# Performance work log

Measured on AMD Instinct MI355X. Metric: run time of the kernel, lower is better.

## Reference

```python
import jax, jax.numpy as jnp
import numpy as np

N = 2
GRIDS = [(512, 512), (256, 256), (128, 128), (64, 64), (32, 32)]
STRIDES = [4, 8, 16, 32, 64]
SIZES = [32, 64, 128, 256, 512]
ASPECTS = (0.5, 1.0, 2.0)
A = len(ASPECTS)
IMG_H = IMG_W = 2048
PRE_NMS = 1000      # pre_nms_top_n['testing']
POST_NMS = 1000     # post_nms_top_n['testing']
NMS_THRESH = 0.7
SCORE_THRESH = 0.0
MIN_SIZE = 1e-3
BBOX_XFORM_CLIP = float(np.log(1000.0 / 16.0))  # torchvision BoxCoder clamp


def _make_anchors():
    """AnchorGenerator.grid_anchors for each level; returns list of [H*W*A, 4]."""
    ar = jnp.asarray(ASPECTS, jnp.float32)
    hr = jnp.sqrt(ar)
    wr = 1.0 / hr
    levels = []
    for (gh, gw), s, size in zip(GRIDS, STRIDES, SIZES):
        ws = wr * size
        hs = hr * size
        base = jnp.round(jnp.stack([-ws, -hs, ws, hs], 1) / 2.0)  # [A,4]
        sx = (jnp.arange(gw) * s).astype(jnp.float32)
        sy = (jnp.arange(gh) * s).astype(jnp.float32)
        yy, xx = jnp.meshgrid(sy, sx, indexing='ij')
        shifts = jnp.stack([xx.ravel(), yy.ravel(), xx.ravel(), yy.ravel()], 1)
        levels.append((shifts[:, None, :] + base[None, :, :]).reshape(-1, 4))
    return levels


def _flatten_obj(o):
    # permute_and_flatten with C=1: [N,A,H,W] -> [N, H*W*A]
    n, ac, h, w = o.shape
    return o.reshape(n, ac, 1, h, w).transpose(0, 3, 4, 1, 2).reshape(n, -1)


def _flatten_box(b):
    # permute_and_flatten with C=4: [N,A*4,H,W] -> [N, H*W*A, 4]
    n, a4, h, w = b.shape
    return b.reshape(n, a4 // 4, 4, h, w).transpose(0, 3, 4, 1, 2).reshape(n, -1, 4)


def _decode(deltas, anchors):
    # BoxCoder.decode with weights (1,1,1,1); deltas [N,M,4], anchors [M,4]
    wa = anchors[:, 2] - anchors[:, 0]
    ha = anchors[:, 3] - anchors[:, 1]
    cxa = anchors[:, 0] + 0.5 * wa
    cya = anchors[:, 1] + 0.5 * ha
    dx, dy = deltas[..., 0], deltas[..., 1]
    dw = jnp.minimum(deltas[..., 2], BBOX_XFORM_CLIP)
    dh = jnp.minimum(deltas[..., 3], BBOX_XFORM_CLIP)
    cx = dx * wa + cxa
    cy = dy * ha + cya
    w = jnp.exp(dw) * wa
    h = jnp.exp(dh) * ha
    return jnp.stack([cx - 0.5 * w, cy - 0.5 * h, cx + 0.5 * w, cy + 0.5 * h], -1)


def _nms_select(boxes, scores, n_out, thresh):
    """Greedy NMS returning fixed n_out (index, valid) pairs. boxes [K,4]."""
    area = jnp.maximum(boxes[:, 2] - boxes[:, 0], 0.0) * jnp.maximum(boxes[:, 3] - boxes[:, 1], 0.0)

    def step(s, _):
        i = jnp.argmax(s)
        valid = s[i] > -jnp.inf
        b = boxes[i]
        lt = jnp.maximum(boxes[:, :2], b[:2])
        rb = jnp.minimum(boxes[:, 2:], b[2:])
        wh = jnp.maximum(rb - lt, 0.0)
        inter = wh[:, 0] * wh[:, 1]
        iou = inter / (area + area[i] - inter + 1e-9)
        s = jnp.where(iou > thresh, -jnp.inf, s).at[i].set(-jnp.inf)
        return s, (i, valid)

    _, (idx, valid) = jax.lax.scan(step, scores, None, length=n_out)
    return idx, valid


def _rpn_forward(objs, dts):
    anchors = _make_anchors()
    b_all, s_all, l_all = [], [], []
    for li, (o, d, a) in enumerate(zip(objs, dts, anchors)):
        of = _flatten_obj(o)            # [N, HWA]
        df = _flatten_box(d)            # [N, HWA, 4]
        props = _decode(df, a)          # [N, HWA, 4]
        k = min(PRE_NMS, of.shape[1])
        ts, ti = jax.lax.top_k(of, k)   # top-k on raw objectness (per level)
        b_all.append(jnp.take_along_axis(props, ti[..., None], 1))
        s_all.append(ts)
        l_all.append(jnp.full((of.shape[0], k), float(li), jnp.float32))
    boxes = jnp.concatenate(b_all, 1)   # [N, K, 4]
    raw = jnp.concatenate(s_all, 1)     # [N, K]
    lvl = jnp.concatenate(l_all, 1)     # [N, K]

    def per_image(bx, rs, lv):
        sc = jax.nn.sigmoid(rs)
        x1 = jnp.clip(bx[:, 0], 0.0, IMG_W)
        y1 = jnp.clip(bx[:, 1], 0.0, IMG_H)
        x2 = jnp.clip(bx[:, 2], 0.0, IMG_W)
        y2 = jnp.clip(bx[:, 3], 0.0, IMG_H)
        bx = jnp.stack([x1, y1, x2, y2], 1)
        keep = ((x2 - x1) >= MIN_SIZE) & ((y2 - y1) >= MIN_SIZE) & (sc > SCORE_THRESH)
        ms = jnp.where(keep, sc, -jnp.inf)
        off = lv * (IMG_W + IMG_H + 1.0)  # batched_nms level offset
        idx, valid = _nms_select(jax.lax.stop_gradient(bx + off[:, None]),
                                 jax.lax.stop_gradient(ms), POST_NMS, NMS_THRESH)
        v = valid.astype(bx.dtype)
        ob = bx[idx] * v[:, None]
        os = sc[idx] * v
        return jnp.concatenate([ob, os[:, None]], 1)  # [POST_NMS, 5]

    return jax.vmap(per_image)(boxes, raw, lvl)       # [N, POST_NMS, 5]


def setup_inputs() -> dict:
    key = jax.random.key(0)
    ks = jax.random.split(key, 10)
    inp = {}
    for i, (gh, gw) in enumerate(GRIDS):
        inp[f"obj{i}"] = jax.random.normal(ks[i], (N, A, gh, gw), jnp.float32)
        inp[f"box{i}"] = jax.random.normal(ks[5 + i], (N, A * 4, gh, gw), jnp.float32) * 0.5
    return inp


def reference(obj0, obj1, obj2, obj3, obj4, box0, box1, box2, box3, box4):
    return _rpn_forward([obj0, obj1, obj2, obj3, obj4],
                        [box0, box1, box2, box3, box4])
```

## Files before the change

kernel.cpp:

```cpp
#include <hip/hip_runtime.h>
#include <cmath>

#pragma clang fp contract(off)

typedef unsigned int u32;
typedef unsigned short u16;
typedef unsigned long long u64;

#define K_PER_LVL 1000
#define KTOT 5000
#define NIMG 2
#define BINS 16384
#define BIN_SHIFT 18
#define SEGW (BINS / 256)
#define EQ_CAP 2048
#define ECAP 32768
#define LECAP 24576
#define CBUF 1024
#define RNK_IB 512
#define RNK_JB 250
#define RNK_NJ (KTOT / RNK_JB)
#define RNK_TILES 200
#define EDGE_TILES 820

__constant__ int c_LG[5] = {512, 256, 128, 64, 32};
__constant__ int c_LS[5] = {4, 8, 16, 32, 64};
__constant__ int c_LZ[5] = {32, 64, 128, 256, 512};
__constant__ int c_LM[5] = {786432, 196608, 49152, 12288, 3072};

struct Ptrs { const float* o[5]; const float* b[5]; };

__device__ inline u32 fkey(float f) {
    u32 u = __float_as_uint(f);
    return (u & 0x80000000u) ? ~u : (u | 0x80000000u);
}

__global__ __launch_bounds__(256) void k_zero(u32* __restrict__ z, int nwords) {
    int i = blockIdx.x * 256 + threadIdx.x;
    int stride = gridDim.x * 256;
    for (; i < nwords; i += stride) z[i] = 0;
}

__global__ __launch_bounds__(256) void k_hist(Ptrs P, u32* __restrict__ hist) {
    int p = blockIdx.y; int l = p % 5; int n = p / 5;
    int M4 = c_LM[l] >> 2;
    const float4* base = (const float4*)(P.o[l] + (size_t)n * c_LM[l]);
    __shared__ u32 lh[BINS];
    for (int i = threadIdx.x; i < BINS; i += 256) lh[i] = 0;
    __syncthreads();
    int stride = gridDim.x * 256;
    for (int i = blockIdx.x * 256 + threadIdx.x; i < M4; i += stride) {
        float4 v = base[i];
        atomicAdd(&lh[fkey(v.x) >> BIN_SHIFT], 1u);
        atomicAdd(&lh[fkey(v.y) >> BIN_SHIFT], 1u);
        atomicAdd(&lh[fkey(v.z) >> BIN_SHIFT], 1u);
        atomicAdd(&lh[fkey(v.w) >> BIN_SHIFT], 1u);
    }
    __syncthreads();
    for (int i = threadIdx.x; i < BINS; i += 256) {
        u32 c = lh[i];
        if (c) atomicAdd(&hist[p * BINS + i], c);
    }
}

__global__ __launch_bounds__(256) void k_resolve(const u32* __restrict__ hist,
                                                 int* __restrict__ binB, int* __restrict__ kneed,
                                                 int* __restrict__ g0) {
    int p = blockIdx.x, t = threadIdx.x;
    __shared__ u32 seg[256];
    __shared__ u32 tail[SEGW];
    __shared__ int sgS; __shared__ u32 GS;
    u32 s = 0;
    const u32* hb = hist + p * BINS;
    int base = t * SEGW;
    for (int q = 0; q < SEGW; ++q) s += hb[base + q];
    seg[t] = s;
    __syncthreads();
    if (t == 0) {
        u32 G = 0; int sg = 255;
        for (; sg > 0; --sg) {
            if (G + seg[sg] >= (u32)K_PER_LVL) break;
            G += seg[sg];
        }
        sgS = sg; GS = G;
    }
    __syncthreads();
    int sg = sgS;
    if (t < SEGW) tail[t] = hb[sg * SEGW + t];
    __syncthreads();
    if (t == 0) {
        u32 G = GS; int B = sg * SEGW;
        for (int b = SEGW - 1; b >= 0; --b) {
            u32 c = tail[b];
            if (G + c >= (u32)K_PER_LVL) { B = sg * SEGW + b; break; }
            G += c;
        }
        binB[p] = B;
        kneed[p] = K_PER_LVL - (int)G;
        g0[p] = (int)G;
    }
}

__global__ __launch_bounds__(256) void k_compact(Ptrs P, const int* __restrict__ binB,
                                                 u32* gcnt, u32* ecnt,
                                                 int* __restrict__ sel, u64* __restrict__ eq) {
    int p = blockIdx.y; int l = p % 5; int n = p / 5;
    int M4 = c_LM[l] >> 2; int gg = c_LM[l] / 3;
    const float4* base = (const float4*)(P.o[l] + (size_t)n * c_LM[l]);
    int B = binB[p];
    __shared__ u32 lsel[CBUF];
    __shared__ u64 leq[CBUF];
    __shared__ u32 cSel, cEq, baseSel, baseEq;
    if (threadIdx.x == 0) { cSel = 0; cEq = 0; }
    __syncthreads();
    int stride = gridDim.x * 256;
    for (int i4 = blockIdx.x * 256 + threadIdx.x; i4 < M4; i4 += stride) {
        float4 v = base[i4];
        float vv[4] = {v.x, v.y, v.z, v.w};
        #pragma unroll
        for (int q = 0; q < 4; ++q) {
            u32 k = fkey(vv[q]);
            int bin = (int)(k >> BIN_SHIFT);
            if (bin < B) continue;
            int i = i4 * 4 + q;
            int a = i / gg; int pix = i - a * gg; int m = pix * 3 + a;
            if (bin > B) {
                u32 t = atomicAdd(&cSel, 1u);
                if (t < CBUF) lsel[t] = (u32)m;
                else { u32 pos = atomicAdd(&gcnt[p], 1u); sel[p * K_PER_LVL + pos] = m; }
            } else {
                u64 pk = ((u64)k << 20) | (u64)(0xFFFFFu ^ (u32)m);
                u32 t = atomicAdd(&cEq, 1u);
                if (t < CBUF) leq[t] = pk;
                else { u32 e = atomicAdd(&ecnt[p], 1u); if (e < EQ_CAP) eq[(size_t)p * EQ_CAP + e] = pk; }
            }
        }
    }
    __syncthreads();
    if (threadIdx.x == 0) {
        u32 ns = cSel < CBUF ? cSel : CBUF;
        u32 ne = cEq < CBUF ? cEq : CBUF;
        baseSel = ns ? atomicAdd(&gcnt[p], ns) : 0u;
        baseEq  = ne ? atomicAdd(&ecnt[p], ne) : 0u;
    }
    __syncthreads();
    u32 ns = cSel < CBUF ? cSel : CBUF;
    u32 ne = cEq < CBUF ? cEq : CBUF;
    for (u32 i = threadIdx.x; i < ns; i += 256) sel[p * K_PER_LVL + baseSel + i] = (int)lsel[i];
    for (u32 i = threadIdx.x; i < ne; i += 256) {
        u32 slot = baseEq + i;
        if (slot < EQ_CAP) eq[(size_t)p * EQ_CAP + slot] = leq[i];
    }
}

__global__ __launch_bounds__(256) void k_eqsel(const u32* __restrict__ ecnt, const int* __restrict__ kneed,
                                               const int* __restrict__ g0,
                                               const u64* __restrict__ eq, int* __restrict__ sel) {
    int p = blockIdx.x, t = threadIdx.x;
    int E = (int)ecnt[p]; if (E > EQ_CAP) E = EQ_CAP;
    int KF = kneed[p]; int G0 = g0[p];
    __shared__ u64 a[EQ_CAP];
    for (int i = t; i < E; i += 256) a[i] = eq[(size_t)p * EQ_CAP + i];
    __syncthreads();
    u64 mine[8]; int rk[8];
    #pragma unroll
    for (int q = 0; q < 8; ++q) {
        int i = t + q * 256;
        mine[q] = (i < E) ? a[i] : 0ULL;
        rk[q] = 0;
    }
    for (int j = 0; j < E; ++j) {
        u64 v = a[j];
        #pragma unroll
        for (int q = 0; q < 8; ++q) rk[q] += (v > mine[q]) ? 1 : 0;
    }
    #pragma unroll
    for (int q = 0; q < 8; ++q) {
        int i = t + q * 256;
        if (i < E && rk[q] < KF) {
            int m = (int)(0xFFFFFu ^ (u32)(mine[q] & 0xFFFFFu));
            sel[p * K_PER_LVL + G0 + rk[q]] = m;
        }
    }
}

__global__ void k_feat(Ptrs P, const int* __restrict__ sel, u64* __restrict__ key64,
                       float* __restrict__ csc, float* __restrict__ cbox, float* __restrict__ cobox) {
    int tid = blockIdx.x * 256 + threadIdx.x;
    if (tid >= NIMG * KTOT) return;
    int p = tid / K_PER_LVL, s = tid - p * K_PER_LVL;
    int n = p / 5, l = p % 5;
    int G = c_LG[l], S = c_LS[l], Z = c_LZ[l];
    int gg = G * G;
    int m = sel[p * K_PER_LVL + s];
    int a = m % 3; int pix = m / 3; int h = pix / G; int w = pix - h * G;

    const float ars[3] = {0.5f, 1.0f, 2.0f};
    float ar = ars[a];
    float hr = sqrtf(ar), wr = 1.0f / hr;
    float wsz = wr * (float)Z, hsz = hr * (float)Z;
    float bx1 = rintf(-0.5f * wsz), by1 = rintf(-0.5f * hsz);
    float bx2 = rintf(0.5f * wsz),  by2 = rintf(0.5f * hsz);
    float sx = (float)(w * S), sy = (float)(h * S);
    float ax1 = sx + bx1, ay1 = sy + by1, ax2 = sx + bx2, ay2 = sy + by2;
    float wa = ax2 - ax1, ha = ay2 - ay1;
    float cxa = ax1 + 0.5f * wa, cya = ay1 + 0.5f * ha;

    const float* bb = P.b[l] + (size_t)n * 12 * gg;
    float dx = bb[(a * 4 + 0) * gg + pix];
    float dy = bb[(a * 4 + 1) * gg + pix];
    const float CLIPV = 4.135166556742356f;
    float dw = fminf(bb[(a * 4 + 2) * gg + pix], CLIPV);
    float dh = fminf(bb[(a * 4 + 3) * gg + pix], CLIPV);
    float cx = dx * wa + cxa, cy = dy * ha + cya;
    float ww = expf(dw) * wa, hh = expf(dh) * ha;
    float x1 = cx - 0.5f * ww, y1 = cy - 0.5f * hh;
    float x2 = cx + 0.5f * ww, y2 = cy + 0.5f * hh;
    x1 = fminf(fmaxf(x1, 0.f), 2048.f);
    y1 = fminf(fmaxf(y1, 0.f), 2048.f);
    x2 = fminf(fmaxf(x2, 0.f), 2048.f);
    y2 = fminf(fmaxf(y2, 0.f), 2048.f);

    float raw = P.o[l][(size_t)n * 3 * gg + a * gg + pix];
    float sc = 1.0f / (1.0f + expf(-raw));
    bool keep = (x2 - x1 >= 1e-3f) && (y2 - y1 >= 1e-3f) && (sc > 0.0f);

    int slot = n * KTOT + l * K_PER_LVL + s;
    u32 tb = ((u32)l << 20) | (u32)m;
    u32 kk = keep ? fkey(raw) : 0u;
    key64[slot] = ((u64)kk << 23) | (u64)(tb ^ 0x7FFFFFu);

    csc[slot] = keep ? sc : -INFINITY;
    cbox[slot * 4 + 0] = x1; cbox[slot * 4 + 1] = y1;
    cbox[slot * 4 + 2] = x2; cbox[slot * 4 + 3] = y2;
    float off = 4097.0f * (float)l;
    cobox[slot * 4 + 0] = x1 + off; cobox[slot * 4 + 1] = y1 + off;
    cobox[slot * 4 + 2] = x2 + off; cobox[slot * 4 + 3] = y2 + off;
}

__global__ __launch_bounds__(256) void k_redge(const u64* __restrict__ key64, u32* __restrict__ rpart,
                                               const float* __restrict__ cobox,
                                               u32* __restrict__ gE, u32* __restrict__ gPairs) {
    int n = blockIdx.y;
    int x = blockIdx.x;
    __shared__ u64 kj[RNK_JB];
    __shared__ float cb[64][4];
    if (x < RNK_TILES) {
        int i0 = (x / 20) * RNK_IB;
        int j0 = (x % 20) * RNK_JB;
        const u64* kb = key64 + (size_t)n * KTOT;
        for (int t = threadIdx.x; t < RNK_JB; t += 256) kj[t] = kb[j0 + t];
        __syncthreads();
        int i1 = i0 + threadIdx.x, i2 = i1 + 256;
        u64 k1 = (i1 < KTOT) ? kb[i1] : ~0ULL;
        u64 k2 = (i2 < KTOT) ? kb[i2] : ~0ULL;
        u32 r1 = 0, r2 = 0;
        #pragma unroll 10
        for (int j = 0; j < RNK_JB; ++j) {
            u64 v = kj[j];
            r1 += (v > k1) ? 1u : 0u;
            r2 += (v > k2) ? 1u : 0u;
        }
        u32* rp = rpart + (size_t)(x % 20) * (NIMG * KTOT) + n * KTOT;
        if (i1 < KTOT) rp[i1] = r1;
        if (i2 < KTOT) rp[i2] = r2;
        return;
    }
    int e = x - RNK_TILES, bi = 0;
    while (true) { int c = 79 - 4 * bi; if (e < c) break; e -= c; ++bi; }
    int bj = 4 * bi + e;
    int i = bi * 256 + threadIdx.x;
    int j0 = bj * 64;
    if (threadIdx.x < 64) {
        int jl = j0 + threadIdx.x;
        if (jl < KTOT) {
            cb[threadIdx.x][0] = cobox[(size_t)(n * KTOT + jl) * 4 + 0];
            cb[threadIdx.x][1] = cobox[(size_t)(n * KTOT + jl) * 4 + 1];
            cb[threadIdx.x][2] = cobox[(size_t)(n * KTOT + jl) * 4 + 2];
            cb[threadIdx.x][3] = cobox[(size_t)(n * KTOT + jl) * 4 + 3];
        } else {
            cb[threadIdx.x][0] = 0.f; cb[threadIdx.x][1] = 0.f;
            cb[threadIdx.x][2] = 0.f; cb[threadIdx.x][3] = 0.f;
        }
    }
    __syncthreads();
    if (i >= KTOT) return;
    float x1 = cobox[(size_t)(n * KTOT + i) * 4 + 0];
    float y1 = cobox[(size_t)(n * KTOT + i) * 4 + 1];
    float x2 = cobox[(size_t)(n * KTOT + i) * 4 + 2];
    float y2 = cobox[(size_t)(n * KTOT + i) * 4 + 3];
    float areai = fmaxf(x2 - x1, 0.f) * fmaxf(y2 - y1, 0.f);
    int lim = KTOT - j0; if (lim > 64) lim = 64;
    for (int jj = 0; jj < lim; ++jj) {
        int j = j0 + jj;
        if (j <= i) continue;
        float bx1 = cb[jj][0], by1 = cb[jj][1], bx2 = cb[jj][2], by2 = cb[jj][3];
        float areaj = fmaxf(bx2 - bx1, 0.f) * fmaxf(by2 - by1, 0.f);
        float ltx = fmaxf(x1, bx1), lty = fmaxf(y1, by1);
        float rbx = fminf(x2, bx2), rby = fminf(y2, by2);
        float iw = fmaxf(rbx - ltx, 0.f), ih = fmaxf(rby - lty, 0.f);
        float inter = iw * ih;
        float iou = inter / (areai + areaj - inter + 1e-9f);
        if (iou > 0.7f) {
            u32 pos = atomicAdd(&gE[n], 1u);
            if (pos < ECAP) gPairs[(size_t)n * ECAP + pos] = ((u32)i << 13) | (u32)j;
        }
    }
}

__global__ __launch_bounds__(256) void k_scat(const u32* __restrict__ rpart, const float* __restrict__ csc,
                       const float* __restrict__ cbox,
                       float* __restrict__ ssc, float* __restrict__ sbox, u32* __restrict__ rankArr) {
    int n = blockIdx.y;
    int i = blockIdx.x * 256 + threadIdx.x;
    if (i >= KTOT) return;
    int idx = n * KTOT + i;
    u32 rank = 0;
    #pragma unroll
    for (int jb = 0; jb < RNK_NJ; ++jb) rank += rpart[(size_t)jb * (NIMG * KTOT) + idx];
    rankArr[idx] = rank;
    int src = idx, dst = n * KTOT + (int)rank;
    ssc[dst] = csc[src];
    sbox[dst * 4 + 0] = cbox[src * 4 + 0]; sbox[dst * 4 + 1] = cbox[src * 4 + 1];
    sbox[dst * 4 + 2] = cbox[src * 4 + 2]; sbox[dst * 4 + 3] = cbox[src * 4 + 3];
}

__global__ __launch_bounds__(256, 1) void k_nms(const float* __restrict__ ssc,
                      const float* __restrict__ sbox, const u32* __restrict__ rankArr,
                      const u32* __restrict__ gE, const u32* __restrict__ gPairs,
                      u16* __restrict__ gEdges, float* __restrict__ out) {
    int n = blockIdx.x, tid = threadIdx.x;
    int lane = tid & 63, wv = tid >> 6;
    __shared__ u32 cnt[KTOT];
    __shared__ u32 offs[KTOT + 1];
    __shared__ u16 edges[LECAP];
    __shared__ u32 rem32[160];
    __shared__ u32 colLo[64], colHi[64];
    __shared__ u32 scanb[256];
    __shared__ int picksS;

    for (int i = tid; i < KTOT; i += 256) cnt[i] = 0;
    if (tid < 160) rem32[tid] = 0xFFFFFFFFu;
    __syncthreads();
    for (int w = wv; w < 79; w += 4) {
        int i = w * 64 + lane;
        bool dead = (i >= KTOT) || !(ssc[n * KTOT + i] > -INFINITY);
        u64 db = __ballot(dead);
        if (lane == 0) { rem32[2 * w] = (u32)db; rem32[2 * w + 1] = (u32)(db >> 32); }
    }
    __syncthreads();

    int E = (int)gE[n]; if (E > ECAP) E = ECAP;
    for (int k = tid; k < E; k += 256) {
        u32 p = gPairs[(size_t)n * ECAP + k];
        u32 ra = rankArr[n * KTOT + (p >> 13)], rb = rankArr[n * KTOT + (p & 0x1FFFu)];
        u32 src = ra < rb ? ra : rb;
        atomicAdd(&cnt[src], 1u);
    }
    __syncthreads();
    u32 s = 0; int base = tid * 20;
    if (tid < 250) for (int q = 0; q < 20; ++q) s += cnt[base + q];
    scanb[tid] = s;
    __syncthreads();
    for (int off = 1; off < 256; off <<= 1) {
        u32 v = (tid >= off) ? scanb[tid - off] : 0;
        __syncthreads();
        scanb[tid] += v;
        __syncthreads();
    }
    u32 tbase = (tid == 0) ? 0u : scanb[tid - 1];
    if (tid < 250) {
        u32 run = tbase;
        for (int q = 0; q < 20; ++q) { offs[base + q] = run; run += cnt[base + q]; }
    }
    if (tid == 0) offs[KTOT] = scanb[255];
    __syncthreads();
    for (int i = tid; i < KTOT; i += 256) cnt[i] = 0;
    __syncthreads();
    for (int k = tid; k < E; k += 256) {
        u32 p = gPairs[(size_t)n * ECAP + k];
        u32 ra = rankArr[n * KTOT + (p >> 13)], rb = rankArr[n * KTOT + (p & 0x1FFFu)];
        u32 src = ra < rb ? ra : rb, dst = ra < rb ? rb : ra;
        u32 slot = offs[src] + atomicAdd(&cnt[src], 1u);
        if (slot < LECAP) edges[slot] = (u16)dst;
        else gEdges[(size_t)n * ECAP + slot] = (u16)dst;
    }
    __syncthreads();

    if (wv == 0) {
        int picks = 0;
        for (int w = 0; w < 79 && picks < 1000; ++w) {
            u64 rw = ((u64)rem32[2 * w + 1] << 32) | rem32[2 * w];
            u64 alive = ~rw;
            if (alive == 0ULL) continue;
            int c = w * 64 + lane;
            bool amAlive = ((alive >> lane) & 1ULL) != 0ULL;
            int e0 = 0, e1 = 0;
            if (amAlive) { e0 = (int)offs[c]; e1 = (int)offs[c + 1]; }
            colLo[lane] = 0; colHi[lane] = 0;
            bool anyIntra = false;
            for (int k = e0; k < e1; ++k) {
                int dst = (k < LECAP) ? (int)edges[k] : (int)gEdges[(size_t)n * ECAP + k];
                if ((dst >> 6) == w) {
                    if (lane < 32) atomicOr(&colLo[dst & 63], 1u << lane);
                    else           atomicOr(&colHi[dst & 63], 1u << (lane - 32));
                    anyIntra = true;
                }
            }
            u64 cm;
            if (__ballot(anyIntra) == 0ULL) {
                cm = alive;
            } else {
                u64 col = ((u64)colHi[lane] << 32) | colLo[lane];
                cm = 0ULL;
                for (int e = 0; e < 64; ++e) {
                    if (!((alive >> e) & 1ULL)) continue;
                    u64 ce = __shfl(col, e);
                    if ((cm & ce) == 0ULL) cm |= (1ULL << e);
                }
            }
            int allowed = 1000 - picks;
            int ncom = __popcll(cm);
            while (ncom > allowed) { cm &= ~(1ULL << (63 - __clzll(cm))); --ncom; }
            if ((cm >> lane) & 1ULL) {
                int pos = picks + (int)__popcll(cm & ((1ULL << lane) - 1ULL));
                const float* bp = &sbox[(size_t)(n * KTOT + c) * 4];
                float* op = &out[(n * 1000 + pos) * 5];
                op[0] = bp[0]; op[1] = bp[1]; op[2] = bp[2]; op[3] = bp[3];
                op[4] = ssc[n * KTOT + c];
                for (int k = e0; k < e1; ++k) {
                    int dst = (k < LECAP) ? (int)edges[k] : (int)gEdges[(size_t)n * ECAP + k];
                    atomicOr(&rem32[dst >> 5], 1u << (dst & 31));
                }
            }
            picks += ncom;
        }
        if (lane == 0) picksS = picks;
    }
    __syncthreads();
    int picksF = picksS;
    int basec = (n * 1000 + picksF) * 5, cntz = (1000 - picksF) * 5;
    for (int t = tid; t < cntz; t += 256) out[basec + t] = 0.f;
}

constexpr size_t OFF_HIST   = 0;
constexpr size_t OFF_GCNT   = OFF_HIST + 10 * BINS * 4;
constexpr size_t OFF_ECNT   = OFF_GCNT + 64;
constexpr size_t OFF_GEC    = OFF_ECNT + 64;
constexpr size_t ZERO_WORDS = (10 * BINS * 4 + 192) / 4;
constexpr size_t OFF_BINB   = OFF_GEC + 64;
constexpr size_t OFF_KNEED  = OFF_BINB + 64;
constexpr size_t OFF_G0     = OFF_KNEED + 64;
constexpr size_t OFF_SEL    = OFF_G0 + 64;
constexpr size_t OFF_EQ     = OFF_SEL + 10 * K_PER_LVL * 4;
constexpr size_t OFF_KEY64  = OFF_EQ + (size_t)10 * EQ_CAP * 8;
constexpr size_t OFF_CSC    = OFF_KEY64 + (size_t)NIMG * KTOT * 8;
constexpr size_t OFF_CBOX   = OFF_CSC + (size_t)NIMG * KTOT * 4;
constexpr size_t OFF_COBOX  = OFF_CBOX + (size_t)NIMG * KTOT * 16;
constexpr size_t OFF_SSC    = OFF_COBOX + (size_t)NIMG * KTOT * 16;
constexpr size_t OFF_SBOX   = OFF_SSC + (size_t)NIMG * KTOT * 4;
constexpr size_t OFF_RANK   = OFF_SBOX + (size_t)NIMG * KTOT * 16;
constexpr size_t OFF_PAIRS  = OFF_RANK + (size_t)NIMG * KTOT * 4;
constexpr size_t OFF_ESPILL = OFF_PAIRS + (size_t)NIMG * ECAP * 4;
constexpr size_t OFF_RPART  = OFF_ESPILL + (size_t)NIMG * ECAP * 2;
constexpr size_t WS_NEEDED  = OFF_RPART + (size_t)RNK_NJ * NIMG * KTOT * 4;

extern "C" void kernel_launch(void* const* d_in, const int* in_sizes, int n_in,
                              void* d_out, int out_size, void* d_ws, size_t ws_size,
                              hipStream_t stream) {
    if (ws_size < WS_NEEDED) return;

    bool dictOrder = (in_sizes[1] > in_sizes[0]);
    Ptrs P;
    for (int l = 0; l < 5; ++l) {
        P.o[l] = (const float*)d_in[dictOrder ? (2 * l)     : l];
        P.b[l] = (const float*)d_in[dictOrder ? (2 * l + 1) : (5 + l)];
    }
    char* ws = (char*)d_ws;
    u32*   hist   = (u32*)(ws + OFF_HIST);
    u32*   gcnt   = (u32*)(ws + OFF_GCNT);
    u32*   ecnt   = (u32*)(ws + OFF_ECNT);
    u32*   gec    = (u32*)(ws + OFF_GEC);
    int*   binB   = (int*)(ws + OFF_BINB);
    int*   kneed  = (int*)(ws + OFF_KNEED);
    int*   g0     = (int*)(ws + OFF_G0);
    int*   sel    = (int*)(ws + OFF_SEL);
    u64*   eq     = (u64*)(ws + OFF_EQ);
    u64*   key64  = (u64*)(ws + OFF_KEY64);
    float* csc    = (float*)(ws + OFF_CSC);
    float* cbox   = (float*)(ws + OFF_CBOX);
    float* cobox  = (float*)(ws + OFF_COBOX);
    float* ssc    = (float*)(ws + OFF_SSC);
    float* sbox   = (float*)(ws + OFF_SBOX);
    u32*   rankA  = (u32*)(ws + OFF_RANK);
    u32*   pairs  = (u32*)(ws + OFF_PAIRS);
    u16*   espill = (u16*)(ws + OFF_ESPILL);
    u32*   rpart  = (u32*)(ws + OFF_RPART);
    float* out    = (float*)d_out;

    k_zero<<<dim3(64), 256, 0, stream>>>(hist, (int)ZERO_WORDS);
    k_hist<<<dim3(32, 10), 256, 0, stream>>>(P, hist);
    k_resolve<<<10, 256, 0, stream>>>(hist, binB, kneed, g0);
    k_compact<<<dim3(64, 10), 256, 0, stream>>>(P, binB, gcnt, ecnt, sel, eq);
    k_eqsel<<<10, 256, 0, stream>>>(ecnt, kneed, g0, eq, sel);
    k_feat<<<dim3((NIMG * KTOT + 255) / 256), 256, 0, stream>>>(P, sel, key64, csc, cbox, cobox);
    k_redge<<<dim3(RNK_TILES + EDGE_TILES, NIMG), 256, 0, stream>>>(key64, rpart, cobox, gec, pairs);
    k_scat<<<dim3((KTOT + 255) / 256, NIMG), 256, 0, stream>>>(rpart, csc, cbox, ssc, sbox, rankA);
    k_nms<<<NIMG, 256, 0, stream>>>(ssc, sbox, rankA, gec, pairs, espill, out);
}
```

Before: 199.3 us.

## Fuse RPN pipeline into one cooperative persistent kernel with grid syncs

Replaces the chain of nine kernel launches (zero, histogram, resolve, compact, equal-bin select, feature decode, rank/edge, scatter, NMS) with a single cooperative kernel of 256 blocks that steps through the stages separated by grid-wide barriers. Histogram work is remapped so slices are distributed per level in proportion to level size. The intent is to remove per-launch overhead and inter-kernel gaps on a pipeline made of many small stages. The cost is grid-sync latency, a fixed grid that may underuse the device in some stages, and shared-memory and occupancy limits from merging all stages into one kernel; the old multi-kernel path is kept as a fallback when cooperative launch is unavailable or fails.

```diff
diff --git a/kernel.cpp b/kernel.cpp
--- a/kernel.cpp
+++ b/kernel.cpp
@@ -1,7 +1,10 @@
 #include <hip/hip_runtime.h>
+#include <hip/hip_cooperative_groups.h>
 #include <cmath>
 
 #pragma clang fp contract(off)
+
+namespace cg = cooperative_groups;
 
 typedef unsigned int u32;
 typedef unsigned short u16;
@@ -22,6 +25,8 @@
 #define RNK_NJ (KTOT / RNK_JB)
 #define RNK_TILES 200
 #define EDGE_TILES 820
+#define NTILES (RNK_TILES + EDGE_TILES)
+#define GRID_ALL 256
 
 __constant__ int c_LG[5] = {512, 256, 128, 64, 32};
 __constant__ int c_LS[5] = {4, 8, 16, 32, 64};
@@ -30,169 +35,36 @@
 
 struct Ptrs { const float* o[5]; const float* b[5]; };
 
+struct Args {
+    Ptrs P;
+    u32* hist; u32* gcnt; u32* ecnt; u32* gec;
+    int* binB; int* kneed; int* g0; int* sel;
+    u64* eq; u64* key64;
+    float* csc; float* cbox; float* cobox;
+    u32* pairs; u16* espill; u32* rpart;
+    float* out;
+};
+
 __device__ inline u32 fkey(float f) {
     u32 u = __float_as_uint(f);
     return (u & 0x80000000u) ? ~u : (u | 0x80000000u);
 }
 
-__global__ __launch_bounds__(256) void k_zero(u32* __restrict__ z, int nwords) {
-    int i = blockIdx.x * 256 + threadIdx.x;
-    int stride = gridDim.x * 256;
-    for (; i < nwords; i += stride) z[i] = 0;
-}
-
-__global__ __launch_bounds__(256) void k_hist(Ptrs P, u32* __restrict__ hist) {
-    int p = blockIdx.y; int l = p % 5; int n = p / 5;
-    int M4 = c_LM[l] >> 2;
-    const float4* base = (const float4*)(P.o[l] + (size_t)n * c_LM[l]);
-    __shared__ u32 lh[BINS];
-    for (int i = threadIdx.x; i < BINS; i += 256) lh[i] = 0;
-    __syncthreads();
-    int stride = gridDim.x * 256;
-    for (int i = blockIdx.x * 256 + threadIdx.x; i < M4; i += stride) {
-        float4 v = base[i];
-        atomicAdd(&lh[fkey(v.x) >> BIN_SHIFT], 1u);
-        atomicAdd(&lh[fkey(v.y) >> BIN_SHIFT], 1u);
-        atomicAdd(&lh[fkey(v.z) >> BIN_SHIFT], 1u);
-        atomicAdd(&lh[fkey(v.w) >> BIN_SHIFT], 1u);
-    }
-    __syncthreads();
-    for (int i = threadIdx.x; i < BINS; i += 256) {
-        u32 c = lh[i];
-        if (c) atomicAdd(&hist[p * BINS + i], c);
-    }
-}
-
-__global__ __launch_bounds__(256) void k_resolve(const u32* __restrict__ hist,
-                                                 int* __restrict__ binB, int* __restrict__ kneed,
-                                                 int* __restrict__ g0) {
-    int p = blockIdx.x, t = threadIdx.x;
-    __shared__ u32 seg[256];
-    __shared__ u32 tail[SEGW];
-    __shared__ int sgS; __shared__ u32 GS;
-    u32 s = 0;
-    const u32* hb = hist + p * BINS;
-    int base = t * SEGW;
-    for (int q = 0; q < SEGW; ++q) s += hb[base + q];
-    seg[t] = s;
-    __syncthreads();
-    if (t == 0) {
-        u32 G = 0; int sg = 255;
-        for (; sg > 0; --sg) {
-            if (G + seg[sg] >= (u32)K_PER_LVL) break;
-            G += seg[sg];
-        }
-        sgS = sg; GS = G;
-    }
-    __syncthreads();
-    int sg = sgS;
-    if (t < SEGW) tail[t] = hb[sg * SEGW + t];
-    __syncthreads();
-    if (t == 0) {
-        u32 G = GS; int B = sg * SEGW;
-        for (int b = SEGW - 1; b >= 0; --b) {
-            u32 c = tail[b];
-            if (G + c >= (u32)K_PER_LVL) { B = sg * SEGW + b; break; }
-            G += c;
-        }
-        binB[p] = B;
-        kneed[p] = K_PER_LVL - (int)G;
-        g0[p] = (int)G;
-    }
-}
-
-__global__ __launch_bounds__(256) void k_compact(Ptrs P, const int* __restrict__ binB,
-                                                 u32* gcnt, u32* ecnt,
-                                                 int* __restrict__ sel, u64* __restrict__ eq) {
-    int p = blockIdx.y; int l = p % 5; int n = p / 5;
-    int M4 = c_LM[l] >> 2; int gg = c_LM[l] / 3;
-    const float4* base = (const float4*)(P.o[l] + (size_t)n * c_LM[l]);
-    int B = binB[p];
-    __shared__ u32 lsel[CBUF];
-    __shared__ u64 leq[CBUF];
-    __shared__ u32 cSel, cEq, baseSel, baseEq;
-    if (threadIdx.x == 0) { cSel = 0; cEq = 0; }
-    __syncthreads();
-    int stride = gridDim.x * 256;
-    for (int i4 = blockIdx.x * 256 + threadIdx.x; i4 < M4; i4 += stride) {
-        float4 v = base[i4];
-        float vv[4] = {v.x, v.y, v.z, v.w};
-        #pragma unroll
-        for (int q = 0; q < 4; ++q) {
-            u32 k = fkey(vv[q]);
-            int bin = (int)(k >> BIN_SHIFT);
-            if (bin < B) continue;
-            int i = i4 * 4 + q;
-            int a = i / gg; int pix = i - a * gg; int m = pix * 3 + a;
-            if (bin > B) {
-                u32 t = atomicAdd(&cSel, 1u);
-                if (t < CBUF) lsel[t] = (u32)m;
-                else { u32 pos = atomicAdd(&gcnt[p], 1u); sel[p * K_PER_LVL + pos] = m; }
-            } else {
-                u64 pk = ((u64)k << 20) | (u64)(0xFFFFFu ^ (u32)m);
-                u32 t = atomicAdd(&cEq, 1u);
-                if (t < CBUF) leq[t] = pk;
-                else { u32 e = atomicAdd(&ecnt[p], 1u); if (e < EQ_CAP) eq[(size_t)p * EQ_CAP + e] = pk; }
-            }
-        }
-    }
-    __syncthreads();
-    if (threadIdx.x == 0) {
-        u32 ns = cSel < CBUF ? cSel : CBUF;
-        u32 ne = cEq < CBUF ? cEq : CBUF;
-        baseSel = ns ? atomicAdd(&gcnt[p], ns) : 0u;
-        baseEq  = ne ? atomicAdd(&ecnt[p], ne) : 0u;
-    }
-    __syncthreads();
-    u32 ns = cSel < CBUF ? cSel : CBUF;
-    u32 ne = cEq < CBUF ? cEq : CBUF;
-    for (u32 i = threadIdx.x; i < ns; i += 256) sel[p * K_PER_LVL + baseSel + i] = (int)lsel[i];
-    for (u32 i = threadIdx.x; i < ne; i += 256) {
-        u32 slot = baseEq + i;
-        if (slot < EQ_CAP) eq[(size_t)p * EQ_CAP + slot] = leq[i];
-    }
-}
-
-__global__ __launch_bounds__(256) void k_eqsel(const u32* __restrict__ ecnt, const int* __restrict__ kneed,
-                                               const int* __restrict__ g0,
-                                               const u64* __restrict__ eq, int* __restrict__ sel) {
-    int p = blockIdx.x, t = threadIdx.x;
-    int E = (int)ecnt[p]; if (E > EQ_CAP) E = EQ_CAP;
-    int KF = kneed[p]; int G0 = g0[p];
-    __shared__ u64 a[EQ_CAP];
-    for (int i = t; i < E; i += 256) a[i] = eq[(size_t)p * EQ_CAP + i];
-    __syncthreads();
-    u64 mine[8]; int rk[8];
-    #pragma unroll
-    for (int q = 0; q < 8; ++q) {
-        int i = t + q * 256;
-        mine[q] = (i < E) ? a[i] : 0ULL;
-        rk[q] = 0;
-    }
-    for (int j = 0; j < E; ++j) {
-        u64 v = a[j];
-        #pragma unroll
-        for (int q = 0; q < 8; ++q) rk[q] += (v > mine[q]) ? 1 : 0;
-    }
-    #pragma unroll
-    for (int q = 0; q < 8; ++q) {
-        int i = t + q * 256;
-        if (i < E && rk[q] < KF) {
-            int m = (int)(0xFFFFFu ^ (u32)(mine[q] & 0xFFFFFu));
-            sel[p * K_PER_LVL + G0 + rk[q]] = m;
-        }
-    }
-}
-
-__global__ void k_feat(Ptrs P, const int* __restrict__ sel, u64* __restrict__ key64,
-                       float* __restrict__ csc, float* __restrict__ cbox, float* __restrict__ cobox) {
-    int tid = blockIdx.x * 256 + threadIdx.x;
-    if (tid >= NIMG * KTOT) return;
-    int p = tid / K_PER_LVL, s = tid - p * K_PER_LVL;
+__device__ inline void histMap(int b, int& p, int& sl, int& nsl) {
+    int n = b >> 7, r = b & 127;
+    int l, s0, c;
+    if (r < 94)       { l = 0; s0 = 0;   c = 94; }
+    else if (r < 118) { l = 1; s0 = 94;  c = 24; }
+    else if (r < 124) { l = 2; s0 = 118; c = 6;  }
+    else if (r < 126) { l = 3; s0 = 124; c = 2;  }
+    else              { l = 4; s0 = 126; c = 2;  }
+    p = n * 5 + l; sl = r - s0; nsl = c;
+}
+
+__device__ inline void featOneM(const Args& A, int p, int s, int m) {
     int n = p / 5, l = p % 5;
     int G = c_LG[l], S = c_LS[l], Z = c_LZ[l];
     int gg = G * G;
-    int m = sel[p * K_PER_LVL + s];
     int a = m % 3; int pix = m / 3; int h = pix / G; int w = pix - h * G;
 
     const float ars[3] = {0.5f, 1.0f, 2.0f};
@@ -206,7 +78,7 @@
     float wa = ax2 - ax1, ha = ay2 - ay1;
     float cxa = ax1 + 0.5f * wa, cya = ay1 + 0.5f * ha;
 
-    const float* bb = P.b[l] + (size_t)n * 12 * gg;
+    const float* bb = A.P.b[l] + (size_t)n * 12 * gg;
     float dx = bb[(a * 4 + 0) * gg + pix];
     float dy = bb[(a * 4 + 1) * gg + pix];
     const float CLIPV = 4.135166556742356f;
@@ -221,227 +93,41 @@
     x2 = fminf(fmaxf(x2, 0.f), 2048.f);
     y2 = fminf(fmaxf(y2, 0.f), 2048.f);
 
-    float raw = P.o[l][(size_t)n * 3 * gg + a * gg + pix];
+    float raw = A.P.o[l][(size_t)n * 3 * gg + a * gg + pix];
     float sc = 1.0f / (1.0f + expf(-raw));
     bool keep = (x2 - x1 >= 1e-3f) && (y2 - y1 >= 1e-3f) && (sc > 0.0f);
 
     int slot = n * KTOT + l * K_PER_LVL + s;
     u32 tb = ((u32)l << 20) | (u32)m;
     u32 kk = keep ? fkey(raw) : 0u;
-    key64[slot] = ((u64)kk << 23) | (u64)(tb ^ 0x7FFFFFu);
-
-    csc[slot] = keep ? sc : -INFINITY;
-    cbox[slot * 4 + 0] = x1; cbox[slot * 4 + 1] = y1;
-    cbox[slot * 4 + 2] = x2; cbox[slot * 4 + 3] = y2;
+    A.key64[slot] = ((u64)kk << 23) | (u64)(tb ^ 0x7FFFFFu);
+
+    A.csc[slot] = keep ? sc : -INFINITY;
+    A.cbox[slot * 4 + 0] = x1; A.cbox[slot * 4 + 1] = y1;
+    A.cbox[slot * 4 + 2] = x2; A.cbox[slot * 4 + 3] = y2;
     float off = 4097.0f * (float)l;
-    cobox[slot * 4 + 0] = x1 + off; cobox[slot * 4 + 1] = y1 + off;
-    cobox[slot * 4 + 2] = x2 + off; cobox[slot * 4 + 3] = y2 + off;
-}
-
-__global__ __launch_bounds__(256) void k_redge(const u64* __restrict__ key64, u32* __restrict__ rpart,
-                                               const float* __restrict__ cobox,
-                                               u32* __restrict__ gE, u32* __restrict__ gPairs) {
-    int n = blockIdx.y;
-    int x = blockIdx.x;
-    __shared__ u64 kj[RNK_JB];
-    __shared__ float cb[64][4];
-    if (x < RNK_TILES) {
-        int i0 = (x / 20) * RNK_IB;
-        int j0 = (x % 20) * RNK_JB;
-        const u64* kb = key64 + (size_t)n * KTOT;
-        for (int t = threadIdx.x; t < RNK_JB; t += 256) kj[t] = kb[j0 + t];
-        __syncthreads();
-        int i1 = i0 + threadIdx.x, i2 = i1 + 256;
-        u64 k1 = (i1 < KTOT) ? kb[i1] : ~0ULL;
-        u64 k2 = (i2 < KTOT) ? kb[i2] : ~0ULL;
-        u32 r1 = 0, r2 = 0;
-        #pragma unroll 10
-        for (int j = 0; j < RNK_JB; ++j) {
-            u64 v = kj[j];
-            r1 += (v > k1) ? 1u : 0u;
-            r2 += (v > k2) ? 1u : 0u;
-        }
-        u32* rp = rpart + (size_t)(x % 20) * (NIMG * KTOT) + n * KTOT;
-        if (i1 < KTOT) rp[i1] = r1;
-        if (i2 < KTOT) rp[i2] = r2;
-        return;
-    }
-    int e = x - RNK_TILES, bi = 0;
-    while (true) { int c = 79 - 4 * bi; if (e < c) break; e -= c; ++bi; }
-    int bj = 4 * bi + e;
-    int i = bi * 256 + threadIdx.x;
-    int j0 = bj * 64;
-    if (threadIdx.x < 64) {
-        int jl = j0 + threadIdx.x;
-        if (jl < KTOT) {
-            cb[threadIdx.x][0] = cobox[(size_t)(n * KTOT + jl) * 4 + 0];
-            cb[threadIdx.x][1] = cobox[(size_t)(n * KTOT + jl) * 4 + 1];
-            cb[threadIdx.x][2] = cobox[(size_t)(n * KTOT + jl) * 4 + 2];
-            cb[threadIdx.x][3] = cobox[(size_t)(n * KTOT + jl) * 4 + 3];
-        } else {
-            cb[threadIdx.x][0] = 0.f; cb[threadIdx.x][1] = 0.f;
-            cb[threadIdx.x][2] = 0.f; cb[threadIdx.x][3] = 0.f;
-        }
-    }
-    __syncthreads();
-    if (i >= KTOT) return;
-    float x1 = cobox[(size_t)(n * KTOT + i) * 4 + 0];
-    float y1 = cobox[(size_t)(n * KTOT + i) * 4 + 1];
-    float x2 = cobox[(size_t)(n * KTOT + i) * 4 + 2];
-    float y2 = cobox[(size_t)(n * KTOT + i) * 4 + 3];
-    float areai = fmaxf(x2 - x1, 0.f) * fmaxf(y2 - y1, 0.f);
-    int lim = KTOT - j0; if (lim > 64) lim = 64;
-    for (int jj = 0; jj < lim; ++jj) {
-        int j = j0 + jj;
-        if (j <= i) continue;
-        float bx1 = cb[jj][0], by1 = cb[jj][1], bx2 = cb[jj][2], by2 = cb[jj][3];
-        float areaj = fmaxf(bx2 - bx1, 0.f) * fmaxf(by2 - by1, 0.f);
-        float ltx = fmaxf(x1, bx1), lty = fmaxf(y1, by1);
-        float rbx = fminf(x2, bx2), rby = fminf(y2, by2);
-        float iw = fmaxf(rbx - ltx, 0.f), ih = fmaxf(rby - lty, 0.f);
-        float inter = iw * ih;
-        float iou = inter / (areai + areaj - inter + 1e-9f);
-        if (iou > 0.7f) {
-            u32 pos = atomicAdd(&gE[n], 1u);
-            if (pos < ECAP) gPairs[(size_t)n * ECAP + pos] = ((u32)i << 13) | (u32)j;
-        }
-    }
-}
-
-__global__ __launch_bounds__(256) void k_scat(const u32* __restrict__ rpart, const float* __restrict__ csc,
-                       const float* __restrict__ cbox,
-                       float* __restrict__ ssc, float* __restrict__ sbox, u32* __restrict__ rankArr) {
-    int n = blockIdx.y;
-    int i = blockIdx.x * 256 + threadIdx.x;
-    if (i >= KTOT) return;
-    int idx = n * KTOT + i;
-    u32 rank = 0;
-    #pragma unroll
-    for (int jb = 0; jb < RNK_NJ; ++jb) rank += rpart[(size_t)jb * (NIMG * KTOT) + idx];
-    rankArr[idx] = rank;
-    int src = idx, dst = n * KTOT + (int)rank;
-    ssc[dst] = csc[src];
-    sbox[dst * 4 + 0] = cbox[src * 4 + 0]; sbox[dst * 4 + 1] = cbox[src * 4 + 1];
-    sbox[dst * 4 + 2] = cbox[src * 4 + 2]; sbox[dst * 4 + 3] = cbox[src * 4 + 3];
-}
-
-__global__ __launch_bounds__(256, 1) void k_nms(const float* __restrict__ ssc,
-                      const float* __restrict__ sbox, const u32* __restrict__ rankArr,
-                      const u32* __restrict__ gE, const u32* __restrict__ gPairs,
-                      u16* __restrict__ gEdges, float* __restrict__ out) {
-    int n = blockIdx.x, tid = threadIdx.x;
-    int lane = tid & 63, wv = tid >> 6;
-    __shared__ u32 cnt[KTOT];
-    __shared__ u32 offs[KTOT + 1];
-    __shared__ u16 edges[LECAP];
-    __shared__ u32 rem32[160];
-    __shared__ u32 colLo[64], colHi[64];
-    __shared__ u32 scanb[256];
-    __shared__ int picksS;
-
-    for (int i = tid; i < KTOT; i += 256) cnt[i] = 0;
-    if (tid < 160) rem32[tid] = 0xFFFFFFFFu;
-    __syncthreads();
-    for (int w = wv; w < 79; w += 4) {
-        int i = w * 64 + lane;
-        bool dead = (i >= KTOT) || !(ssc[n * KTOT + i] > -INFINITY);
-        u64 db = __ballot(dead);
-        if (lane == 0) { rem32[2 * w] = (u32)db; rem32[2 * w + 1] = (u32)(db >> 32); }
-    }
-    __syncthreads();
-
-    int E = (int)gE[n]; if (E > ECAP) E = ECAP;
-    for (int k = tid; k < E; k += 256) {
-        u32 p = gPairs[(size_t)n * ECAP + k];
-        u32 ra = rankArr[n * KTOT + (p >> 13)], rb = rankArr[n * KTOT + (p & 0x1FFFu)];
-        u32 src = ra < rb ? ra : rb;
-        atomicAdd(&cnt[src], 1u);
-    }
-    __syncthreads();
-    u32 s = 0; int base = tid * 20;
-    if (tid < 250) for (int q = 0; q < 20; ++q) s += cnt[base + q];
-    scanb[tid] = s;
-    __syncthreads();
-    for (int off = 1; off < 256; off <<= 1) {
-        u32 v = (tid >= off) ? scanb[tid - off] : 0;
-        __syncthreads();
-        scanb[tid] += v;
-        __syncthreads();
-    }
-    u32 tbase = (tid == 0) ? 0u : scanb[tid - 1];
-    if (tid < 250) {
-        u32 run = tbase;
-        for (int q = 0; q < 20; ++q) { offs[base + q] = run; run += cnt[base + q]; }
-    }
-    if (tid == 0) offs[KTOT] = scanb[255];
-    __syncthreads();
-    for (int i = tid; i < KTOT; i += 256) cnt[i] = 0;
-    __syncthreads();
-    for (int k = tid; k < E; k += 256) {
-        u32 p = gPairs[(size_t)n * ECAP + k];
-        u32 ra = rankArr[n * KTOT + (p >> 13)], rb = rankArr[n * KTOT + (p & 0x1FFFu)];
-        u32 src = ra < rb ? ra : rb, dst = ra < rb ? rb : ra;
-        u32 slot = offs[src] + atomicAdd(&cnt[src], 1u);
-        if (slot < LECAP) edges[slot] = (u16)dst;
-        else gEdges[(size_t)n * ECAP + slot] = (u16)dst;
-    }
-    __syncthreads();
-
-    if (wv == 0) {
-        int picks = 0;
-        for (int w = 0; w < 79 && picks < 1000; ++w) {
-            u64 rw = ((u64)rem32[2 * w + 1] << 32) | rem32[2 * w];
-            u64 alive = ~rw;
-            if (alive == 0ULL) continue;
-            int c = w * 64 + lane;
-            bool amAlive = ((alive >> lane) & 1ULL) != 0ULL;
-            int e0 = 0, e1 = 0;
-            if (amAlive) { e0 = (int)offs[c]; e1 = (int)offs[c + 1]; }
-            colLo[lane] = 0; colHi[lane] = 0;
-            bool anyIntra = false;
-            for (int k = e0; k < e1; ++k) {
-                int dst = (k < LECAP) ? (int)edges[k] : (int)gEdges[(size_t)n * ECAP + k];
-                if ((dst >> 6) == w) {
-                    if (lane < 32) atomicOr(&colLo[dst & 63], 1u << lane);
-                    else           atomicOr(&colHi[dst & 63], 1u << (lane - 32));
-                    anyIntra = true;
-                }
-            }
-            u64 cm;
-            if (__ballot(anyIntra) == 0ULL) {
-                cm = alive;
-            } else {
-                u64 col = ((u64)colHi[lane] << 32) | colLo[lane];
-                cm = 0ULL;
-                for (int e = 0; e < 64; ++e) {
-                    if (!((alive >> e) & 1ULL)) continue;
-                    u64 ce = __shfl(col, e);
-                    if ((cm & ce) == 0ULL) cm |= (1ULL << e);
-                }
-            }
-            int allowed = 1000 - picks;
-            int ncom = __popcll(cm);
-            while (ncom > allowed) { cm &= ~(1ULL << (63 - __clzll(cm))); --ncom; }
-            if ((cm >> lane) & 1ULL) {
-                int pos = picks + (int)__popcll(cm & ((1ULL << lane) - 1ULL));
-                const float* bp = &sbox[(size_t)(n * KTOT + c) * 4];
-                float* op = &out[(n * 1000 + pos) * 5];
-                op[0] = bp[0]; op[1] = bp[1]; op[2] = bp[2]; op[3] = bp[3];
-                op[4] = ssc[n * KTOT + c];
-                for (int k = e0; k < e1; ++k) {
-                    int dst = (k < LECAP) ? (int)edges[k] : (int)gEdges[(size_t)n * ECAP + k];
-                    atomicOr(&rem32[dst >> 5], 1u << (dst & 31));
-                }
-            }
-            picks += ncom;
-        }
-        if (lane == 0) picksS = picks;
-    }
-    __syncthreads();
-    int picksF = picksS;
-    int basec = (n * 1000 + picksF) * 5, cntz = (1000 - picksF) * 5;
-    for (int t = tid; t < cntz; t += 256) out[basec + t] = 0.f;
-}
+    A.cobox[slot * 4 + 0] = x1 + off; A.cobox[slot * 4 + 1] = y1 + off;
+    A.cobox[slot * 4 + 2] = x2 + off; A.cobox[slot * 4 + 3] = y2 + off;
+}
+
+struct __align__(16) SmHist { u32 lh[BINS]; };
+struct __align__(16) SmResolve { u32 seg[256]; u32 tail[SEGW]; int sgS; u32 GS; };
+struct __align__(16) SmCompact { u64 leq[CBUF]; u32 lsel[CBUF]; u32 cSel, cEq, baseSel, baseEq; };
+struct __align__(16) SmEqsel { u64 a[EQ_CAP]; };
+struct __align__(16) SmRedge { u64 kj[RNK_JB]; float cb[64][4]; };
+struct __align__(16) SmNms {
+    u32 cnt[KTOT];
+    u32 offs[KTOT + 1];
+    u32 rem32[160];
+    u32 colLo[64], colHi[64];
+    u32 scanb[256];
+    int picksS;
+    u16 rankL[KTOT];
+    u16 invL[KTOT];
+    u16 edges[LECAP];
+};
+union SmAll { SmHist h; SmResolve r; SmCompact c; SmEqsel e; SmRedge g; SmNms n; };
+static_assert(sizeof(SmAll) <= 160 * 1024, "LDS union too large");
 
 constexpr size_t OFF_HIST   = 0;
 constexpr size_t OFF_GCNT   = OFF_HIST + 10 * BINS * 4;
@@ -465,6 +151,713 @@
 constexpr size_t OFF_RPART  = OFF_ESPILL + (size_t)NIMG * ECAP * 2;
 constexpr size_t WS_NEEDED  = OFF_RPART + (size_t)RNK_NJ * NIMG * KTOT * 4;
 
+__global__ __launch_bounds__(256, 1) void k_all(Args A) {
+    cg::grid_group grid = cg::this_grid();
+    __shared__ SmAll sm;
+    const int tid = threadIdx.x;
+    const int b = blockIdx.x;
+
+    {
+        const int nw = (int)ZERO_WORDS;
+        for (int i = b * 256 + tid; i < nw; i += GRID_ALL * 256) A.hist[i] = 0;
+    }
+    grid.sync();
+
+    {
+        int p, sl, nsl; histMap(b, p, sl, nsl);
+        int l = p % 5, n = p / 5;
+        int M4 = c_LM[l] >> 2;
+        const float4* base = (const float4*)(A.P.o[l] + (size_t)n * c_LM[l]);
+        for (int i = tid; i < BINS; i += 256) sm.h.lh[i] = 0;
+        __syncthreads();
+        for (int i = sl * 256 + tid; i < M4; i += nsl * 256) {
+            float4 v = base[i];
+            atomicAdd(&sm.h.lh[fkey(v.x) >> BIN_SHIFT], 1u);
+            atomicAdd(&sm.h.lh[fkey(v.y) >> BIN_SHIFT], 1u);
+            atomicAdd(&sm.h.lh[fkey(v.z) >> BIN_SHIFT], 1u);
+            atomicAdd(&sm.h.lh[fkey(v.w) >> BIN_SHIFT], 1u);
+        }
+        __syncthreads();
+        for (int i = tid; i < BINS; i += 256) {
+            u32 c = sm.h.lh[i];
+            if (c) atomicAdd(&A.hist[p * BINS + i], c);
+        }
+    }
+    grid.sync();
+
+    if (b < 10) {
+        int p = b, t = tid;
+        u32 s = 0;
+        const u32* hb = A.hist + p * BINS;
+        int base0 = t * SEGW;
+        for (int q = 0; q < SEGW; ++q) s += hb[base0 + q];
+        sm.r.seg[t] = s;
+        __syncthreads();
+        if (t == 0) {
+            u32 G = 0; int sg = 255;
+            for (; sg > 0; --sg) {
+                if (G + sm.r.seg[sg] >= (u32)K_PER_LVL) break;
+                G += sm.r.seg[sg];
+            }
+            sm.r.sgS = sg; sm.r.GS = G;
+        }
+        __syncthreads();
+        int sg = sm.r.sgS;
+        if (t < SEGW) sm.r.tail[t] = hb[sg * SEGW + t];
+        __syncthreads();
+        if (t == 0) {
+            u32 G = sm.r.GS; int B = sg * SEGW;
+            for (int q = SEGW - 1; q >= 0; --q) {
+                u32 c = sm.r.tail[q];
+                if (G + c >= (u32)K_PER_LVL) { B = sg * SEGW + q; break; }
+                G += c;
+            }
+            A.binB[p] = B;
+            A.kneed[p] = K_PER_LVL - (int)G;
+            A.g0[p] = (int)G;
+        }
+    }
+    grid.sync();
+
+    {
+        int p, sl, nsl; histMap(b, p, sl, nsl);
+        int l = p % 5, n = p / 5;
+        int M4 = c_LM[l] >> 2; int gg = c_LM[l] / 3;
+        const float4* base = (const float4*)(A.P.o[l] + (size_t)n * c_LM[l]);
+        int B = A.binB[p];
+        if (tid == 0) { sm.c.cSel = 0; sm.c.cEq = 0; }
+        __syncthreads();
+        for (int i4 = sl * 256 + tid; i4 < M4; i4 += nsl * 256) {
+            float4 v = base[i4];
+            float vv[4] = {v.x, v.y, v.z, v.w};
+            #pragma unroll
+            for (int q = 0; q < 4; ++q) {
+                u32 k = fkey(vv[q]);
+                int bin = (int)(k >> BIN_SHIFT);
+                if (bin < B) continue;
+                int i = i4 * 4 + q;
+                int a = i / gg; int pix = i - a * gg; int m = pix * 3 + a;
+                if (bin > B) {
+                    u32 t = atomicAdd(&sm.c.cSel, 1u);
+                    if (t < CBUF) sm.c.lsel[t] = (u32)m;
+                    else { u32 pos = atomicAdd(&A.gcnt[p], 1u); A.sel[p * K_PER_LVL + pos] = m; }
+                } else {
+                    u64 pk = ((u64)k << 20) | (u64)(0xFFFFFu ^ (u32)m);
+                    u32 t = atomicAdd(&sm.c.cEq, 1u);
+                    if (t < CBUF) sm.c.leq[t] = pk;
+                    else { u32 e = atomicAdd(&A.ecnt[p], 1u); if (e < EQ_CAP) A.eq[(size_t)p * EQ_CAP + e] = pk; }
+                }
+            }
+        }
+        __syncthreads();
+        if (tid == 0) {
+            u32 ns = sm.c.cSel < CBUF ? sm.c.cSel : CBUF;
+            u32 ne = sm.c.cEq < CBUF ? sm.c.cEq : CBUF;
+            sm.c.baseSel = ns ? atomicAdd(&A.gcnt[p], ns) : 0u;
+            sm.c.baseEq  = ne ? atomicAdd(&A.ecnt[p], ne) : 0u;
+        }
+        __syncthreads();
+        u32 ns = sm.c.cSel < CBUF ? sm.c.cSel : CBUF;
+        u32 ne = sm.c.cEq < CBUF ? sm.c.cEq : CBUF;
+        for (u32 i = tid; i < ns; i += 256) A.sel[p * K_PER_LVL + sm.c.baseSel + i] = (int)sm.c.lsel[i];
+        for (u32 i = tid; i < ne; i += 256) {
+            u32 slot = sm.c.baseEq + i;
+            if (slot < EQ_CAP) A.eq[(size_t)p * EQ_CAP + slot] = sm.c.leq[i];
+        }
+    }
+    grid.sync();
+
+    if (b < 10) {
+        int p = b, t = tid;
+        int E = (int)A.ecnt[p]; if (E > EQ_CAP) E = EQ_CAP;
+        int KF = A.kneed[p]; int G0 = A.g0[p];
+        for (int i = t; i < E; i += 256) sm.e.a[i] = A.eq[(size_t)p * EQ_CAP + i];
+        __syncthreads();
+        u64 mine[8]; int rk[8];
+        #pragma unroll
+        for (int q = 0; q < 8; ++q) {
+            int i = t + q * 256;
+            mine[q] = (i < E) ? sm.e.a[i] : 0ULL;
+            rk[q] = 0;
+        }
+        for (int j = 0; j < E; ++j) {
+            u64 v = sm.e.a[j];
+            #pragma unroll
+            for (int q = 0; q < 8; ++q) rk[q] += (v > mine[q]) ? 1 : 0;
+        }
+        #pragma unroll
+        for (int q = 0; q < 8; ++q) {
+            int i = t + q * 256;
+            if (i < E && rk[q] < KF) {
+                int m = (int)(0xFFFFFu ^ (u32)(mine[q] & 0xFFFFFu));
+                featOneM(A, p, G0 + rk[q], m);
+            }
+        }
+    } else {
+        for (int idx = (b - 10) * 256 + tid; idx < 10 * K_PER_LVL; idx += (GRID_ALL - 10) * 256) {
+            int p = idx / K_PER_LVL, s = idx - p * K_PER_LVL;
+            if (s < A.g0[p]) featOneM(A, p, s, A.sel[p * K_PER_LVL + s]);
+        }
+    }
+    grid.sync();
+
+    for (int tile = b; tile < NIMG * NTILES; tile += GRID_ALL) {
+        int n = tile / NTILES;
+        int x = tile - n * NTILES;
+        if (x < RNK_TILES) {
+            int i0 = (x / 20) * RNK_IB;
+            int j0 = (x % 20) * RNK_JB;
+            const u64* kb = A.key64 + (size_t)n * KTOT;
+            for (int t = tid; t < RNK_JB; t += 256) sm.g.kj[t] = kb[j0 + t];
+            __syncthreads();
+            int i1 = i0 + tid, i2 = i1 + 256;
+            u64 k1 = (i1 < KTOT) ? kb[i1] : ~0ULL;
+            u64 k2 = (i2 < KTOT) ? kb[i2] : ~0ULL;
+            u32 r1 = 0, r2 = 0;
+            #pragma unroll 10
+            for (int j = 0; j < RNK_JB; ++j) {
+                u64 v = sm.g.kj[j];
+                r1 += (v > k1) ? 1u : 0u;
+                r2 += (v > k2) ? 1u : 0u;
+            }
+            u32* rp = A.rpart + (size_t)(x % 20) * (NIMG * KTOT) + n * KTOT;
+            if (i1 < KTOT) rp[i1] = r1;
+            if (i2 < KTOT) rp[i2] = r2;
+        } else {
+            int e = x - RNK_TILES, bi = 0;
+            while (true) { int c = 79 - 4 * bi; if (e < c) break; e -= c; ++bi; }
+            int bj = 4 * bi + e;
+            int i = bi * 256 + tid;
+            int j0 = bj * 64;
+            if (tid < 64) {
+                int jl = j0 + tid;
+                if (jl < KTOT) {
+                    sm.g.cb[tid][0] = A.cobox[(size_t)(n * KTOT + jl) * 4 + 0];
+                    sm.g.cb[tid][1] = A.cobox[(size_t)(n * KTOT + jl) * 4 + 1];
+                    sm.g.cb[tid][2] = A.cobox[(size_t)(n * KTOT + jl) * 4 + 2];
+                    sm.g.cb[tid][3] = A.cobox[(size_t)(n * KTOT + jl) * 4 + 3];
+                } else {
+                    sm.g.cb[tid][0] = 0.f; sm.g.cb[tid][1] = 0.f;
+                    sm.g.cb[tid][2] = 0.f; sm.g.cb[tid][3] = 0.f;
+                }
+            }
+            __syncthreads();
+            if (i < KTOT) {
+                float x1 = A.cobox[(size_t)(n * KTOT + i) * 4 + 0];
+                float y1 = A.cobox[(size_t)(n * KTOT + i) * 4 + 1];
+                float x2 = A.cobox[(size_t)(n * KTOT + i) * 4 + 2];
+                float y2 = A.cobox[(size_t)(n * KTOT + i) * 4 + 3];
+                float areai = fmaxf(x2 - x1, 0.f) * fmaxf(y2 - y1, 0.f);
+                int lim = KTOT - j0; if (lim > 64) lim = 64;
+                for (int jj = 0; jj < lim; ++jj) {
+                    int j = j0 + jj;
+                    if (j <= i) continue;
+                    float bx1 = sm.g.cb[jj][0], by1 = sm.g.cb[jj][1];
+                    float bx2 = sm.g.cb[jj][2], by2 = sm.g.cb[jj][3];
+                    float areaj = fmaxf(bx2 - bx1, 0.f) * fmaxf(by2 - by1, 0.f);
+                    float ltx = fmaxf(x1, bx1), lty = fmaxf(y1, by1);
+                    float rbx = fminf(x2, bx2), rby = fminf(y2, by2);
+                    float iw = fmaxf(rbx - ltx, 0.f), ih = fmaxf(rby - lty, 0.f);
+                    float inter = iw * ih;
+                    float iou = inter / (areai + areaj - inter + 1e-9f);
+                    if (iou > 0.7f) {
+                        u32 pos = atomicAdd(&A.gec[n], 1u);
+                        if (pos < ECAP) A.pairs[(size_t)n * ECAP + pos] = ((u32)i << 13) | (u32)j;
+                    }
+                }
+            }
+        }
+        __syncthreads();
+    }
+    grid.sync();
+
+    if (b >= NIMG) return;
+    {
+        int n = b;
+        int lane = tid & 63, wv = tid >> 6;
+        SmNms& S = sm.n;
+
+        for (int i = tid; i < KTOT; i += 256) S.cnt[i] = 0;
+        if (tid < 160) S.rem32[tid] = 0;
+        __syncthreads();
+
+        for (int i = tid; i < KTOT; i += 256) {
+            u32 r = 0;
+            #pragma unroll
+            for (int jb = 0; jb < RNK_NJ; ++jb)
+                r += A.rpart[(size_t)jb * (NIMG * KTOT) + n * KTOT + i];
+            S.rankL[i] = (u16)r;
+            S.invL[r] = (u16)i;
+            if (!(A.csc[n * KTOT + i] > -INFINITY))
+                atomicOr(&S.rem32[r >> 5], 1u << (r & 31));
+        }
+        __syncthreads();
+        if (tid == 0) {
+            S.rem32[156] |= 0xFFFFFF00u;
+            S.rem32[157] = 0xFFFFFFFFu;
+            S.rem32[158] = 0xFFFFFFFFu;
+            S.rem32[159] = 0xFFFFFFFFu;
+        }
+
+        int E = (int)A.gec[n]; if (E > ECAP) E = ECAP;
+        for (int k = tid; k < E; k += 256) {
+            u32 pr = A.pairs[(size_t)n * ECAP + k];
+            u32 ra = S.rankL[pr >> 13], rb = S.rankL[pr & 0x1FFFu];
+            u32 src = ra < rb ? ra : rb;
+            atomicAdd(&S.cnt[src], 1u);
+        }
+        __syncthreads();
+        u32 s0 = 0; int base0 = tid * 20;
+        if (tid < 250) for (int q = 0; q < 20; ++q) s0 += S.cnt[base0 + q];
+        S.scanb[tid] = s0;
+        __syncthreads();
+        for (int off = 1; off < 256; off <<= 1) {
+            u32 v = (tid >= off) ? S.scanb[tid - off] : 0;
+            __syncthreads();
+            S.scanb[tid] += v;
+            __syncthreads();
+        }
+        u32 tbase = (tid == 0) ? 0u : S.scanb[tid - 1];
+        if (tid < 250) {
+            u32 run = tbase;
+            for (int q = 0; q < 20; ++q) { S.offs[base0 + q] = run; run += S.cnt[base0 + q]; }
+        }
+        if (tid == 0) S.offs[KTOT] = S.scanb[255];
+        __syncthreads();
+        for (int i = tid; i < KTOT; i += 256) S.cnt[i] = 0;
+        __syncthreads();
+        for (int k = tid; k < E; k += 256) {
+            u32 pr = A.pairs[(size_t)n * ECAP + k];
+            u32 ra = S.rankL[pr >> 13], rb = S.rankL[pr & 0x1FFFu];
+            u32 src = ra < rb ? ra : rb, dst = ra < rb ? rb : ra;
+            u32 slot = S.offs[src] + atomicAdd(&S.cnt[src], 1u);
+            if (slot < LECAP) S.edges[slot] = (u16)dst;
+            else A.espill[(size_t)n * ECAP + slot] = (u16)dst;
+        }
+        __syncthreads();
+
+        if (wv == 0) {
+            int picks = 0;
+            for (int w = 0; w < 79 && picks < 1000; ++w) {
+                u64 rw = ((u64)S.rem32[2 * w + 1] << 32) | S.rem32[2 * w];
+                u64 alive = ~rw;
+                if (alive == 0ULL) continue;
+                int c = w * 64 + lane;
+                bool amAlive = ((alive >> lane) & 1ULL) != 0ULL;
+                int e0 = 0, e1 = 0;
+                if (amAlive) { e0 = (int)S.offs[c]; e1 = (int)S.offs[c + 1]; }
+                S.colLo[lane] = 0; S.colHi[lane] = 0;
+                bool anyIntra = false;
+                for (int k = e0; k < e1; ++k) {
+                    int dst = (k < LECAP) ? (int)S.edges[k] : (int)A.espill[(size_t)n * ECAP + k];
+                    if ((dst >> 6) == w) {
+                        if (lane < 32) atomicOr(&S.colLo[dst & 63], 1u << lane);
+                        else           atomicOr(&S.colHi[dst & 63], 1u << (lane - 32));
+                        anyIntra = true;
+                    }
+                }
+                u64 cm;
+                if (__ballot(anyIntra) == 0ULL) {
+                    cm = alive;
+                } else {
+                    u64 col = ((u64)S.colHi[lane] << 32) | S.colLo[lane];
+                    cm = 0ULL;
+                    for (int e2 = 0; e2 < 64; ++e2) {
+                        if (!((alive >> e2) & 1ULL)) continue;
+                        u64 ce = __shfl(col, e2);
+                        if ((cm & ce) == 0ULL) cm |= (1ULL << e2);
+                    }
+                }
+                int allowed = 1000 - picks;
+                int ncom = __popcll(cm);
+                while (ncom > allowed) { cm &= ~(1ULL << (63 - __clzll(cm))); --ncom; }
+                if ((cm >> lane) & 1ULL) {
+                    int pos = picks + (int)__popcll(cm & ((1ULL << lane) - 1ULL));
+                    int orig = (int)S.invL[c];
+                    const float* bp = &A.cbox[(size_t)(n * KTOT + orig) * 4];
+                    float* op = &A.out[(n * 1000 + pos) * 5];
+                    op[0] = bp[0]; op[1] = bp[1]; op[2] = bp[2]; op[3] = bp[3];
+                    op[4] = A.csc[n * KTOT + orig];
+                    for (int k = e0; k < e1; ++k) {
+                        int dst = (k < LECAP) ? (int)S.edges[k] : (int)A.espill[(size_t)n * ECAP + k];
+                        atomicOr(&S.rem32[dst >> 5], 1u << (dst & 31));
+                    }
+                }
+                picks += ncom;
+            }
+            if (lane == 0) S.picksS = picks;
+        }
+        __syncthreads();
+        int picksF = S.picksS;
+        int basec = (n * 1000 + picksF) * 5, cntz = (1000 - picksF) * 5;
+        for (int t2 = tid; t2 < cntz; t2 += 256) A.out[basec + t2] = 0.f;
+    }
+}
+
+__global__ __launch_bounds__(256) void k_zero(u32* __restrict__ z, int nwords) {
+    int i = blockIdx.x * 256 + threadIdx.x;
+    int stride = gridDim.x * 256;
+    for (; i < nwords; i += stride) z[i] = 0;
+}
+
+__global__ __launch_bounds__(256) void k_hist(Ptrs P, u32* __restrict__ hist) {
+    int p = blockIdx.y; int l = p % 5; int n = p / 5;
+    int M4 = c_LM[l] >> 2;
+    const float4* base = (const float4*)(P.o[l] + (size_t)n * c_LM[l]);
+    __shared__ u32 lh[BINS];
+    for (int i = threadIdx.x; i < BINS; i += 256) lh[i] = 0;
+    __syncthreads();
+    int stride = gridDim.x * 256;
+    for (int i = blockIdx.x * 256 + threadIdx.x; i < M4; i += stride) {
+        float4 v = base[i];
+        atomicAdd(&lh[fkey(v.x) >> BIN_SHIFT], 1u);
+        atomicAdd(&lh[fkey(v.y) >> BIN_SHIFT], 1u);
+        atomicAdd(&lh[fkey(v.z) >> BIN_SHIFT], 1u);
+        atomicAdd(&lh[fkey(v.w) >> BIN_SHIFT], 1u);
+    }
+    __syncthreads();
+    for (int i = threadIdx.x; i < BINS; i += 256) {
+        u32 c = lh[i];
+        if (c) atomicAdd(&hist[p * BINS + i], c);
+    }
+}
+
+__global__ __launch_bounds__(256) void k_resolve(const u32* __restrict__ hist,
+                                                 int* __restrict__ binB, int* __restrict__ kneed,
+                                                 int* __restrict__ g0) {
+    int p = blockIdx.x, t = threadIdx.x;
+    __shared__ u32 seg[256];
+    __shared__ u32 tail[SEGW];
+    __shared__ int sgS; __shared__ u32 GS;
+    u32 s = 0;
+    const u32* hb = hist + p * BINS;
+    int base = t * SEGW;
+    for (int q = 0; q < SEGW; ++q) s += hb[base + q];
+    seg[t] = s;
+    __syncthreads();
+    if (t == 0) {
+        u32 G = 0; int sg = 255;
+        for (; sg > 0; --sg) {
+            if (G + seg[sg] >= (u32)K_PER_LVL) break;
+            G += seg[sg];
+        }
+        sgS = sg; GS = G;
+    }
+    __syncthreads();
+    int sg = sgS;
+    if (t < SEGW) tail[t] = hb[sg * SEGW + t];
+    __syncthreads();
+    if (t == 0) {
+        u32 G = GS; int B = sg * SEGW;
+        for (int q = SEGW - 1; q >= 0; --q) {
+            u32 c = tail[q];
+            if (G + c >= (u32)K_PER_LVL) { B = sg * SEGW + q; break; }
+            G += c;
+        }
+        binB[p] = B;
+        kneed[p] = K_PER_LVL - (int)G;
+        g0[p] = (int)G;
+    }
+}
+
+__global__ __launch_bounds__(256) void k_compact(Ptrs P, const int* __restrict__ binB,
+                                                 u32* gcnt, u32* ecnt,
+                                                 int* __restrict__ sel, u64* __restrict__ eq) {
+    int p = blockIdx.y; int l = p % 5; int n = p / 5;
+    int M4 = c_LM[l] >> 2; int gg = c_LM[l] / 3;
+    const float4* base = (const float4*)(P.o[l] + (size_t)n * c_LM[l]);
+    int B = binB[p];
+    __shared__ u32 lsel[CBUF];
+    __shared__ u64 leq[CBUF];
+    __shared__ u32 cSel, cEq, baseSel, baseEq;
+    if (threadIdx.x == 0) { cSel = 0; cEq = 0; }
+    __syncthreads();
+    int stride = gridDim.x * 256;
+    for (int i4 = blockIdx.x * 256 + threadIdx.x; i4 < M4; i4 += stride) {
+        float4 v = base[i4];
+        float vv[4] = {v.x, v.y, v.z, v.w};
+        #pragma unroll
+        for (int q = 0; q < 4; ++q) {
+            u32 k = fkey(vv[q]);
+            int bin = (int)(k >> BIN_SHIFT);
+            if (bin < B) continue;
+            int i = i4 * 4 + q;
+            int a = i / gg; int pix = i - a * gg; int m = pix * 3 + a;
+            if (bin > B) {
+                u32 t = atomicAdd(&cSel, 1u);
+                if (t < CBUF) lsel[t] = (u32)m;
+                else { u32 pos = atomicAdd(&gcnt[p], 1u); sel[p * K_PER_LVL + pos] = m; }
+            } else {
+                u64 pk = ((u64)k << 20) | (u64)(0xFFFFFu ^ (u32)m);
+                u32 t = atomicAdd(&cEq, 1u);
+                if (t < CBUF) leq[t] = pk;
+                else { u32 e = atomicAdd(&ecnt[p], 1u); if (e < EQ_CAP) eq[(size_t)p * EQ_CAP + e] = pk; }
+            }
+        }
+    }
+    __syncthreads();
+    if (threadIdx.x == 0) {
+        u32 ns = cSel < CBUF ? cSel : CBUF;
+        u32 ne = cEq < CBUF ? cEq : CBUF;
+        baseSel = ns ? atomicAdd(&gcnt[p], ns) : 0u;
+        baseEq  = ne ? atomicAdd(&ecnt[p], ne) : 0u;
+    }
+    __syncthreads();
+    u32 ns = cSel < CBUF ? cSel : CBUF;
+    u32 ne = cEq < CBUF ? cEq : CBUF;
+    for (u32 i = threadIdx.x; i < ns; i += 256) sel[p * K_PER_LVL + baseSel + i] = (int)lsel[i];
+    for (u32 i = threadIdx.x; i < ne; i += 256) {
+        u32 slot = baseEq + i;
+        if (slot < EQ_CAP) eq[(size_t)p * EQ_CAP + slot] = leq[i];
+    }
+}
+
+__global__ __launch_bounds__(256) void k_eqsel(const u32* __restrict__ ecnt, const int* __restrict__ kneed,
+                                               const int* __restrict__ g0,
+                                               const u64* __restrict__ eq, int* __restrict__ sel) {
+    int p = blockIdx.x, t = threadIdx.x;
+    int E = (int)ecnt[p]; if (E > EQ_CAP) E = EQ_CAP;
+    int KF = kneed[p]; int G0 = g0[p];
+    __shared__ u64 a[EQ_CAP];
+    for (int i = t; i < E; i += 256) a[i] = eq[(size_t)p * EQ_CAP + i];
+    __syncthreads();
+    u64 mine[8]; int rk[8];
+    #pragma unroll
+    for (int q = 0; q < 8; ++q) {
+        int i = t + q * 256;
+        mine[q] = (i < E) ? a[i] : 0ULL;
+        rk[q] = 0;
+    }
+    for (int j = 0; j < E; ++j) {
+        u64 v = a[j];
+        #pragma unroll
+        for (int q = 0; q < 8; ++q) rk[q] += (v > mine[q]) ? 1 : 0;
+    }
+    #pragma unroll
+    for (int q = 0; q < 8; ++q) {
+        int i = t + q * 256;
+        if (i < E && rk[q] < KF) {
+            int m = (int)(0xFFFFFu ^ (u32)(mine[q] & 0xFFFFFu));
+            sel[p * K_PER_LVL + G0 + rk[q]] = m;
+        }
+    }
+}
+
+__global__ void k_feat(Ptrs P, const int* __restrict__ sel, u64* __restrict__ key64,
+                       float* __restrict__ csc, float* __restrict__ cbox, float* __restrict__ cobox) {
+    int tid = blockIdx.x * 256 + threadIdx.x;
+    if (tid >= NIMG * KTOT) return;
+    int p = tid / K_PER_LVL, s = tid - p * K_PER_LVL;
+    Args A;
+    A.P = P; A.sel = (int*)sel; A.key64 = key64; A.csc = csc; A.cbox = cbox; A.cobox = cobox;
+    featOneM(A, p, s, sel[p * K_PER_LVL + s]);
+}
+
+__global__ __launch_bounds__(256) void k_redge(const u64* __restrict__ key64, u32* __restrict__ rpart,
+                                               const float* __restrict__ cobox,
+                                               u32* __restrict__ gE, u32* __restrict__ gPairs) {
+    int n = blockIdx.y;
+    int x = blockIdx.x;
+    __shared__ u64 kj[RNK_JB];
+    __shared__ float cb[64][4];
+    if (x < RNK_TILES) {
+        int i0 = (x / 20) * RNK_IB;
+        int j0 = (x % 20) * RNK_JB;
+        const u64* kb = key64 + (size_t)n * KTOT;
+        for (int t = threadIdx.x; t < RNK_JB; t += 256) kj[t] = kb[j0 + t];
+        __syncthreads();
+        int i1 = i0 + threadIdx.x, i2 = i1 + 256;
+        u64 k1 = (i1 < KTOT) ? kb[i1] : ~0ULL;
+        u64 k2 = (i2 < KTOT) ? kb[i2] : ~0ULL;
+        u32 r1 = 0, r2 = 0;
+        #pragma unroll 10
+        for (int j = 0; j < RNK_JB; ++j) {
+            u64 v = kj[j];
+            r1 += (v > k1) ? 1u : 0u;
+            r2 += (v > k2) ? 1u : 0u;
+        }
+        u32* rp = rpart + (size_t)(x % 20) * (NIMG * KTOT) + n * KTOT;
+        if (i1 < KTOT) rp[i1] = r1;
+        if (i2 < KTOT) rp[i2] = r2;
+        return;
+    }
+    int e = x - RNK_TILES, bi = 0;
+    while (true) { int c = 79 - 4 * bi; if (e < c) break; e -= c; ++bi; }
+    int bj = 4 * bi + e;
+    int i = bi * 256 + threadIdx.x;
+    int j0 = bj * 64;
+    if (threadIdx.x < 64) {
+        int jl = j0 + threadIdx.x;
+        if (jl < KTOT) {
+            cb[threadIdx.x][0] = cobox[(size_t)(n * KTOT + jl) * 4 + 0];
+            cb[threadIdx.x][1] = cobox[(size_t)(n * KTOT + jl) * 4 + 1];
+            cb[threadIdx.x][2] = cobox[(size_t)(n * KTOT + jl) * 4 + 2];
+            cb[threadIdx.x][3] = cobox[(size_t)(n * KTOT + jl) * 4 + 3];
+        } else {
+            cb[threadIdx.x][0] = 0.f; cb[threadIdx.x][1] = 0.f;
+            cb[threadIdx.x][2] = 0.f; cb[threadIdx.x][3] = 0.f;
+        }
+    }
+    __syncthreads();
+    if (i >= KTOT) return;
+    float x1 = cobox[(size_t)(n * KTOT + i) * 4 + 0];
+    float y1 = cobox[(size_t)(n * KTOT + i) * 4 + 1];
+    float x2 = cobox[(size_t)(n * KTOT + i) * 4 + 2];
+    float y2 = cobox[(size_t)(n * KTOT + i) * 4 + 3];
+    float areai = fmaxf(x2 - x1, 0.f) * fmaxf(y2 - y1, 0.f);
+    int lim = KTOT - j0; if (lim > 64) lim = 64;
+    for (int jj = 0; jj < lim; ++jj) {
+        int j = j0 + jj;
+        if (j <= i) continue;
+        float bx1 = cb[jj][0], by1 = cb[jj][1], bx2 = cb[jj][2], by2 = cb[jj][3];
+        float areaj = fmaxf(bx2 - bx1, 0.f) * fmaxf(by2 - by1, 0.f);
+        float ltx = fmaxf(x1, bx1), lty = fmaxf(y1, by1);
+        float rbx = fminf(x2, bx2), rby = fminf(y2, by2);
+        float iw = fmaxf(rbx - ltx, 0.f), ih = fmaxf(rby - lty, 0.f);
+        float inter = iw * ih;
+        float iou = inter / (areai + areaj - inter + 1e-9f);
+        if (iou > 0.7f) {
+            u32 pos = atomicAdd(&gE[n], 1u);
+            if (pos < ECAP) gPairs[(size_t)n * ECAP + pos] = ((u32)i << 13) | (u32)j;
+        }
+    }
+}
+
+__global__ __launch_bounds__(256) void k_scat(const u32* __restrict__ rpart, const float* __restrict__ csc,
+                       const float* __restrict__ cbox,
+                       float* __restrict__ ssc, float* __restrict__ sbox, u32* __restrict__ rankArr) {
+    int n = blockIdx.y;
+    int i = blockIdx.x * 256 + threadIdx.x;
+    if (i >= KTOT) return;
+    int idx = n * KTOT + i;
+    u32 rank = 0;
+    #pragma unroll
+    for (int jb = 0; jb < RNK_NJ; ++jb) rank += rpart[(size_t)jb * (NIMG * KTOT) + idx];
+    rankArr[idx] = rank;
+    int src = idx, dst = n * KTOT + (int)rank;
+    ssc[dst] = csc[src];
+    sbox[dst * 4 + 0] = cbox[src * 4 + 0]; sbox[dst * 4 + 1] = cbox[src * 4 + 1];
+    sbox[dst * 4 + 2] = cbox[src * 4 + 2]; sbox[dst * 4 + 3] = cbox[src * 4 + 3];
+}
+
+__global__ __launch_bounds__(256, 1) void k_nms(const float* __restrict__ ssc,
+                      const float* __restrict__ sbox, const u32* __restrict__ rankArr,
+                      const u32* __restrict__ gE, const u32* __restrict__ gPairs,
+                      u16* __restrict__ gEdges, float* __restrict__ out) {
+    int n = blockIdx.x, tid = threadIdx.x;
+    int lane = tid & 63, wv = tid >> 6;
+    __shared__ u32 cnt[KTOT];
+    __shared__ u32 offs[KTOT + 1];
+    __shared__ u16 edges[LECAP];
+    __shared__ u32 rem32[160];
+    __shared__ u32 colLo[64], colHi[64];
+    __shared__ u32 scanb[256];
+    __shared__ int picksS;
+
+    for (int i = tid; i < KTOT; i += 256) cnt[i] = 0;
+    if (tid < 160) rem32[tid] = 0xFFFFFFFFu;
+    __syncthreads();
+    for (int w = wv; w < 79; w += 4) {
+        int i = w * 64 + lane;
+        bool dead = (i >= KTOT) || !(ssc[n * KTOT + i] > -INFINITY);
+        u64 db = __ballot(dead);
+        if (lane == 0) { rem32[2 * w] = (u32)db; rem32[2 * w + 1] = (u32)(db >> 32); }
+    }
+    __syncthreads();
+
+    int E = (int)gE[n]; if (E > ECAP) E = ECAP;
+    for (int k = tid; k < E; k += 256) {
+        u32 p = gPairs[(size_t)n * ECAP + k];
+        u32 ra = rankArr[n * KTOT + (p >> 13)], rb = rankArr[n * KTOT + (p & 0x1FFFu)];
+        u32 src = ra < rb ? ra : rb;
+        atomicAdd(&cnt[src], 1u);
+    }
+    __syncthreads();
+    u32 s = 0; int base = tid * 20;
+    if (tid < 250) for (int q = 0; q < 20; ++q) s += cnt[base + q];
+    scanb[tid] = s;
+    __syncthreads();
+    for (int off = 1; off < 256; off <<= 1) {
+        u32 v = (tid >= off) ? scanb[tid - off] : 0;
+        __syncthreads();
+        scanb[tid] += v;
+        __syncthreads();
+    }
+    u32 tbase = (tid == 0) ? 0u : scanb[tid - 1];
+    if (tid < 250) {
+        u32 run = tbase;
+        for (int q = 0; q < 20; ++q) { offs[base + q] = run; run += cnt[base + q]; }
+    }
+    if (tid == 0) offs[KTOT] = scanb[255];
+    __syncthreads();
+    for (int i = tid; i < KTOT; i += 256) cnt[i] = 0;
+    __syncthreads();
+    for (int k = tid; k < E; k += 256) {
+        u32 p = gPairs[(size_t)n * ECAP + k];
+        u32 ra = rankArr[n * KTOT + (p >> 13)], rb = rankArr[n * KTOT + (p & 0x1FFFu)];
+        u32 src = ra < rb ? ra : rb, dst = ra < rb ? rb : ra;
+        u32 slot = offs[src] + atomicAdd(&cnt[src], 1u);
+        if (slot < LECAP) edges[slot] = (u16)dst;
+        else gEdges[(size_t)n * ECAP + slot] = (u16)dst;
+    }
+    __syncthreads();
+
+    if (wv == 0) {
+        int picks = 0;
+        for (int w = 0; w < 79 && picks < 1000; ++w) {
+            u64 rw = ((u64)rem32[2 * w + 1] << 32) | rem32[2 * w];
+            u64 alive = ~rw;
+            if (alive == 0ULL) continue;
+            int c = w * 64 + lane;
+            bool amAlive = ((alive >> lane) & 1ULL) != 0ULL;
+            int e0 = 0, e1 = 0;
+            if (amAlive) { e0 = (int)offs[c]; e1 = (int)offs[c + 1]; }
+            colLo[lane] = 0; colHi[lane] = 0;
+            bool anyIntra = false;
+            for (int k = e0; k < e1; ++k) {
+                int dst = (k < LECAP) ? (int)edges[k] : (int)gEdges[(size_t)n * ECAP + k];
+                if ((dst >> 6) == w) {
+                    if (lane < 32) atomicOr(&colLo[dst & 63], 1u << lane);
+                    else           atomicOr(&colHi[dst & 63], 1u << (lane - 32));
+                    anyIntra = true;
+                }
+            }
+            u64 cm;
+            if (__ballot(anyIntra) == 0ULL) {
+                cm = alive;
+            } else {
+                u64 col = ((u64)colHi[lane] << 32) | colLo[lane];
+                cm = 0ULL;
+                for (int e = 0; e < 64; ++e) {
+                    if (!((alive >> e) & 1ULL)) continue;
+                    u64 ce = __shfl(col, e);
+                    if ((cm & ce) == 0ULL) cm |= (1ULL << e);
+                }
+            }
+            int allowed = 1000 - picks;
+            int ncom = __popcll(cm);
+            while (ncom > allowed) { cm &= ~(1ULL << (63 - __clzll(cm))); --ncom; }
+            if ((cm >> lane) & 1ULL) {
+                int pos = picks + (int)__popcll(cm & ((1ULL << lane) - 1ULL));
+                const float* bp = &sbox[(size_t)(n * KTOT + c) * 4];
+                float* op = &out[(n * 1000 + pos) * 5];
+                op[0] = bp[0]; op[1] = bp[1]; op[2] = bp[2]; op[3] = bp[3];
+                op[4] = ssc[n * KTOT + c];
+                for (int k = e0; k < e1; ++k) {
+                    int dst = (k < LECAP) ? (int)edges[k] : (int)gEdges[(size_t)n * ECAP + k];
+                    atomicOr(&rem32[dst >> 5], 1u << (dst & 31));
+                }
+            }
+            picks += ncom;
+        }
+        if (lane == 0) picksS = picks;
+    }
+    __syncthreads();
+    int picksF = picksS;
+    int basec = (n * 1000 + picksF) * 5, cntz = (1000 - picksF) * 5;
+    for (int t = tid; t < cntz; t += 256) out[basec + t] = 0.f;
+}
+
 extern "C" void kernel_launch(void* const* d_in, const int* in_sizes, int n_in,
                               void* d_out, int out_size, void* d_ws, size_t ws_size,
                               hipStream_t stream) {
@@ -498,13 +891,34 @@
     u32*   rpart  = (u32*)(ws + OFF_RPART);
     float* out    = (float*)d_out;
 
-    k_zero<<<dim3(64), 256, 0, stream>>>(hist, (int)ZERO_WORDS);
-    k_hist<<<dim3(32, 10), 256, 0, stream>>>(P, hist);
-    k_resolve<<<10, 256, 0, stream>>>(hist, binB, kneed, g0);
-    k_compact<<<dim3(64, 10), 256, 0, stream>>>(P, binB, gcnt, ecnt, sel, eq);
-    k_eqsel<<<10, 256, 0, stream>>>(ecnt, kneed, g0, eq, sel);
-    k_feat<<<dim3((NIMG * KTOT + 255) / 256), 256, 0, stream>>>(P, sel, key64, csc, cbox, cobox);
-    k_redge<<<dim3(RNK_TILES + EDGE_TILES, NIMG), 256, 0, stream>>>(key64, rpart, cobox, gec, pairs);
-    k_scat<<<dim3((KTOT + 255) / 256, NIMG), 256, 0, stream>>>(rpart, csc, cbox, ssc, sbox, rankA);
-    k_nms<<<NIMG, 256, 0, stream>>>(ssc, sbox, rankA, gec, pairs, espill, out);
-}
+    Args A;
+    A.P = P;
+    A.hist = hist; A.gcnt = gcnt; A.ecnt = ecnt; A.gec = gec;
+    A.binB = binB; A.kneed = kneed; A.g0 = g0; A.sel = sel;
+    A.eq = eq; A.key64 = key64;
+    A.csc = csc; A.cbox = cbox; A.cobox = cobox;
+    A.pairs = pairs; A.espill = espill; A.rpart = rpart;
+    A.out = out;
+
+    int dev = 0, coop = 0;
+    hipGetDevice(&dev);
+    hipDeviceGetAttribute(&coop, hipDeviceAttributeCooperativeLaunch, dev);
+
+    hipError_t err = hipErrorUnknown;
+    if (coop) {
+        void* kargs[] = { (void*)&A };
+        err = hipLaunchCooperativeKernel((const void*)k_all, dim3(GRID_ALL), dim3(256),
+                                         kargs, 0, stream);
+    }
+    if (err != hipSuccess) {
+        k_zero<<<dim3(64), 256, 0, stream>>>(hist, (int)ZERO_WORDS);
+        k_hist<<<dim3(32, 10), 256, 0, stream>>>(P, hist);
+        k_resolve<<<10, 256, 0, stream>>>(hist, binB, kneed, g0);
+        k_compact<<<dim3(64, 10), 256, 0, stream>>>(P, binB, gcnt, ecnt, sel, eq);
+        k_eqsel<<<10, 256, 0, stream>>>(ecnt, kneed, g0, eq, sel);
+        k_feat<<<dim3((NIMG * KTOT + 255) / 256), 256, 0, stream>>>(P, sel, key64, csc, cbox, cobox);
+        k_redge<<<dim3(RNK_TILES + EDGE_TILES, NIMG), 256, 0, stream>>>(key64, rpart, cobox, gec, pairs);
+        k_scat<<<dim3((KTOT + 255) / 256, NIMG), 256, 0, stream>>>(rpart, csc, cbox, ssc, sbox, rankA);
+        k_nms<<<NIMG, 256, 0, stream>>>(ssc, sbox, rankA, gec, pairs, espill, out);
+    }
+}
```

After: 405.7 us. +103.6%, slower.
